# Optimization experiments

Hardware: AMD Instinct MI355X
Metric: run time of the kernel (lower is better)

## Reference

```python
import jax, jax.numpy as jnp
import numpy as np

RADIUS = 0.8
NSAMPLE = 32
EPS = 1e-5  # BatchNorm eps


def _bn(x, gamma, beta, axes):
    # BatchNorm (training-mode batch statistics), channel dim kept via broadcasting
    m = jnp.mean(x, axis=axes, keepdims=True)
    v = jnp.var(x, axis=axes, keepdims=True)
    return (x - m) * jax.lax.rsqrt(v + EPS) * gamma + beta


def setup_inputs() -> dict:
    key = jax.random.key(0)
    ks = jax.random.split(key, 6)
    B, N, P, C, COUT = 4, 8192, 2048, 128, 256
    ffps_xyz = jax.random.uniform(ks[0], (B, P, 3), dtype=jnp.float32) * 2.0 - 1.0
    backbone_xyz = jax.random.uniform(ks[1], (B, N, 3), dtype=jnp.float32) * 2.0 - 1.0
    backbone_features = jax.random.normal(ks[2], (B, C, N), dtype=jnp.float32)
    w_shift = jax.random.normal(ks[3], (3, 3), dtype=jnp.float32) * 0.1
    gamma_shift = jnp.ones((3,), jnp.float32)
    beta_shift = jnp.zeros((3,), jnp.float32)
    w_mlp = jax.random.normal(ks[4], (COUT, 3 + C), dtype=jnp.float32) * 0.05
    gamma_mlp = jnp.ones((COUT,), jnp.float32)
    beta_mlp = jnp.zeros((COUT,), jnp.float32)
    return {
        "ffps_xyz": ffps_xyz,
        "backbone_xyz": backbone_xyz,
        "backbone_features": backbone_features,
        "w_shift": w_shift,
        "gamma_shift": gamma_shift,
        "beta_shift": beta_shift,
        "w_mlp": w_mlp,
        "gamma_mlp": gamma_mlp,
        "beta_mlp": beta_mlp,
    }


def reference(ffps_xyz, backbone_xyz, backbone_features,
              w_shift, gamma_shift, beta_shift,
              w_mlp, gamma_mlp, beta_mlp):
    B, P, _ = ffps_xyz.shape
    N = backbone_xyz.shape[1]

    # ---- shift_layer: Conv1d(3->3, k=1, no bias) + BN1d + ReLU on (B,3,P) ----
    x = jnp.einsum('oc,bpc->bop', w_shift, ffps_xyz)                  # (B,3,P)
    x = _bn(x, gamma_shift[None, :, None], beta_shift[None, :, None], (0, 2))
    new_xyz = jax.nn.relu(x).transpose(0, 2, 1)                       # (B,P,3) query centers

    # ---- QueryAndGroup: ball query (radius, nsample), use_xyz=True ----
    d2 = jnp.sum((new_xyz[:, :, None, :] - backbone_xyz[:, None, :, :]) ** 2, -1)  # (B,P,N)
    within = d2 < (RADIUS * RADIUS)
    # pick the first NSAMPLE in-radius indices (CUDA ball_query semantics)
    keyv = jnp.where(within, jnp.arange(N, dtype=jnp.int32), jnp.int32(N))
    negk, idx = jax.lax.top_k(-keyv, NSAMPLE)                          # smallest keys first
    valid = (-negk) < N
    idx = jnp.where(valid, idx, idx[..., :1])                          # pad with first found idx

    g_xyz = jnp.take_along_axis(backbone_xyz[:, None, :, :], idx[..., None], axis=2)
    g_xyz = g_xyz - new_xyz[:, :, None, :]                             # (B,P,S,3) recentered
    feats = backbone_features.transpose(0, 2, 1)                       # (B,N,C)
    g_f = jnp.take_along_axis(feats[:, None, :, :], idx[..., None], axis=2)  # (B,P,S,C)
    g = jnp.concatenate([g_xyz, g_f], axis=-1)                         # (B,P,S,3+C)

    # ---- mlp: 1x1 conv (3+C -> COUT, no bias) + BN + ReLU ----
    y = jnp.einsum('oc,bpsc->bops', w_mlp, g)                          # (B,COUT,P,S)
    y = _bn(y, gamma_mlp[None, :, None, None], beta_mlp[None, :, None, None], (0, 2, 3))
    y = jax.nn.relu(y)

    # ---- max-pool over neighbor axis, squeeze, transpose ----
    y = jnp.max(y, axis=3)                                             # (B,COUT,P)
    return y.transpose(0, 2, 1)                                        # (B,P,COUT)
```

## Files before the change

kernel.cpp:

```cpp
#include <hip/hip_runtime.h>
#include <math.h>

namespace {
constexpr int B    = 4;
constexpr int N    = 8192;
constexpr int P    = 2048;
constexpr int C    = 128;
constexpr int COUT = 256;
constexpr int NS   = 32;
constexpr int BP   = B * P;
constexpr int BPB  = 2;
constexpr int GRP  = 8;
constexpr int NBLK = BP / (BPB * GRP);

constexpr size_t OFF_FEATT = 0;
constexpr size_t OFF_WSWZ  = 8388608;
constexpr size_t OFF_SSLOT = 8470528;
constexpr size_t OFF_SUMS  = 8471040;
constexpr size_t OFF_NXF   = 8475136;
constexpr size_t OFF_IDX   = 8573440;
constexpr size_t OFF_YMAX  = 9622016;
constexpr size_t WS_NEED   = 18010624;
}

typedef short bf16x8 __attribute__((ext_vector_type(8)));
typedef float f32x4  __attribute__((ext_vector_type(4)));

typedef const __attribute__((address_space(1))) void gas_void;
typedef __attribute__((address_space(3))) void las_void;
#define GLOBAL_LOAD_LDS16(gp, lp) \
    __builtin_amdgcn_global_load_lds((gas_void*)(gp), (las_void*)(lp), 16, 0, 0)

__device__ inline unsigned short f2bf(float f) {
    unsigned u = __float_as_uint(f);
    unsigned r = u + 0x7fffu + ((u >> 16) & 1u);
    return (unsigned short)(r >> 16);
}

__global__ __launch_bounds__(256) void k_prep(const float* __restrict__ ffps,
                                              const float* __restrict__ wsh,
                                              double* __restrict__ sslot,
                                              float* __restrict__ sums) {
#pragma clang fp contract(off)
    int blk = blockIdx.x, t = threadIdx.x;
    if (blk == 8) {
        ((f32x4*)sums)[t & 127] = (f32x4){0.f, 0.f, 0.f, 0.f};
        return;
    }
    __shared__ double red[6][256];
    double w[9];
#pragma unroll
    for (int i = 0; i < 9; i++) w[i] = (double)wsh[i];
    double s[3] = {0, 0, 0}, sq[3] = {0, 0, 0};
#pragma unroll
    for (int i = 0; i < 4; i++) {
        int p = blk * 1024 + t + 256 * i;
        double f0 = (double)ffps[p * 3 + 0];
        double f1 = (double)ffps[p * 3 + 1];
        double f2 = (double)ffps[p * 3 + 2];
#pragma unroll
        for (int o = 0; o < 3; o++) {
            double xo = (w[o * 3 + 0] * f0 + w[o * 3 + 1] * f1) + w[o * 3 + 2] * f2;
            s[o] += xo;
            sq[o] += xo * xo;
        }
    }
#pragma unroll
    for (int o = 0; o < 3; o++) { red[o][t] = s[o]; red[3 + o][t] = sq[o]; }
    for (int off = 128; off > 0; off >>= 1) {
        __syncthreads();
        if (t < off) {
#pragma unroll
            for (int j = 0; j < 6; j++) red[j][t] += red[j][t + off];
        }
    }
    __syncthreads();
    if (t < 6) sslot[blk * 6 + t] = red[t][0];
}

__global__ __launch_bounds__(256) void k_front(const float* __restrict__ ffps,
                                               const float* __restrict__ bbxyz,
                                               const float* __restrict__ feat,
                                               const float* __restrict__ wsh,
                                               const float* __restrict__ gsh,
                                               const float* __restrict__ bsh,
                                               const float* __restrict__ wml,
                                               const double* __restrict__ sslot,
                                               unsigned short* __restrict__ featT,
                                               unsigned short* __restrict__ wswz,
                                               float* __restrict__ nxf,
                                               int* __restrict__ idxo) {
#pragma clang fp contract(off)
    int blk = blockIdx.x, t = threadIdx.x;
    if (blk >= 2048) {
        int rb = blk - 2048;
        if (rb < 2048) {
            __shared__ float tile[64][33];
            int tx = t & 31, ty = t >> 5;
            int n0 = (rb & 255) * 32, c0 = ((rb >> 8) & 1) * 64, b = rb >> 9;
            const float* src = feat + ((size_t)b * C + c0) * N + n0;
#pragma unroll
            for (int j = 0; j < 8; j++) tile[ty + 8 * j][tx] = src[(size_t)(ty + 8 * j) * N + tx];
            __syncthreads();
            int n = t >> 3;
            int k8 = (t & 7) * 8;
            unsigned vv[4];
#pragma unroll
            for (int i = 0; i < 4; i++) {
                unsigned lo = f2bf(tile[k8 + 2 * i][n]);
                unsigned hi = f2bf(tile[k8 + 2 * i + 1][n]);
                vv[i] = lo | (hi << 16);
            }
            *(int4*)&featT[((size_t)b * N + n0 + n) * C + c0 + k8] =
                make_int4((int)vv[0], (int)vv[1], (int)vv[2], (int)vv[3]);
        } else {
            int i = (rb - 2048) * 256 + t;
            int j = i & 7;
            int lane = (i >> 3) & 63;
            int rest = i >> 9;
            int ks = rest % 5, rt = rest / 5;
            int cout = rt * 16 + (lane & 15);
            int k = ks * 32 + (lane >> 4) * 8 + j;
            float v = 0.f;
            if (k < 128) v = wml[cout * 131 + 3 + k];
            else if (k < 131) v = wml[cout * 131 + (k - 128)];
            wswz[i] = f2bf(v);
        }
        return;
    }

    __shared__ double spar[6];
    if (t < 6) {
        double a = 0.0;
        for (int r = 0; r < 8; r++) a += sslot[r * 6 + t];
        spar[t] = a;
    }
    __syncthreads();
    int wv = t >> 6, lane = t & 63;
    int q = blk * 4 + wv;
    int b = q >> 11;
    double f0 = (double)ffps[q * 3 + 0];
    double f1 = (double)ffps[q * 3 + 1];
    double f2 = (double)ffps[q * 3 + 2];
    double qd[3];
#pragma unroll
    for (int o = 0; o < 3; o++) {
        double m  = spar[o] * (1.0 / 8192.0);
        double v  = spar[3 + o] * (1.0 / 8192.0) - m * m;
        double is = 1.0 / sqrt(v + 1e-5);
        double x  = ((double)wsh[o * 3 + 0] * f0 + (double)wsh[o * 3 + 1] * f1) +
                    (double)wsh[o * 3 + 2] * f2;
        double y  = ((x - m) * is) * (double)gsh[o] + (double)bsh[o];
        qd[o] = (y > 0.0) ? y : 0.0;
    }
    double qx = qd[0], qy = qd[1], qz = qd[2];
    if (lane == 0) {
        nxf[q * 3 + 0] = (float)qx;
        nxf[q * 3 + 1] = (float)qy;
        nxf[q * 3 + 2] = (float)qz;
    }
    const double R2 = 0.8 * 0.8;
    {
        double ex = fmax(fmax(qx - 1.0, -1.0 - qx), 0.0);
        double ey = fmax(fmax(qy - 1.0, -1.0 - qy), 0.0);
        double ez = fmax(fmax(qz - 1.0, -1.0 - qz), 0.0);
        if (ex * ex + ey * ey + ez * ez >= R2) {
            if (lane < NS) idxo[q * NS + lane] = 0;
            return;
        }
    }
    const float* base = bbxyz + (size_t)b * N * 3;
    int found = 0, firstn = -1;

    float X0[8], Y0[8], Z0[8], X1[8], Y1[8], Z1[8], X2[8], Y2[8], Z2[8];

    auto loadb = [&](float (&XX)[8], float (&YY)[8], float (&ZZ)[8], int it) {
#pragma unroll
        for (int j = 0; j < 8; j++) {
            int n = it * 512 + j * 64 + lane;
            XX[j] = base[n * 3 + 0];
            YY[j] = base[n * 3 + 1];
            ZZ[j] = base[n * 3 + 2];
        }
    };
    auto proc = [&](float (&XX)[8], float (&YY)[8], float (&ZZ)[8], int it) {
#pragma clang fp contract(off)
#pragma unroll
        for (int j = 0; j < 8; j++) {
            int n = it * 512 + j * 64 + lane;
            double dx = qx - (double)XX[j];
            double dy = qy - (double)YY[j];
            double dz = qz - (double)ZZ[j];
            double d2 = (dx * dx + dy * dy) + dz * dz;
            bool within = d2 < R2;
            unsigned long long mask = __ballot(within);
            if (firstn < 0 && mask != 0ull) firstn = (n - lane) + (__ffsll(mask) - 1);
            if (within) {
                int rank = found + __popcll(mask & ((1ull << lane) - 1ull));
                if (rank < NS) idxo[q * NS + rank] = n;
            }
            found += __popcll(mask);
        }
    };

    loadb(X0, Y0, Z0, 0);
    loadb(X1, Y1, Z1, 1);
    loadb(X2, Y2, Z2, 2);

    for (int itb = 0; itb < 16; itb += 3) {
        proc(X0, Y0, Z0, itb);
        if (found >= NS) break;
        loadb(X0, Y0, Z0, (itb + 3 < 16) ? itb + 3 : 0);
        if (itb + 1 >= 16) break;
        proc(X1, Y1, Z1, itb + 1);
        if (found >= NS) break;
        loadb(X1, Y1, Z1, (itb + 4 < 16) ? itb + 4 : 0);
        if (itb + 2 >= 16) break;
        proc(X2, Y2, Z2, itb + 2);
        if (found >= NS) break;
        loadb(X2, Y2, Z2, (itb + 5 < 16) ? itb + 5 : 0);
    }
    if (found < NS) {
        int padv = (found == 0) ? 0 : firstn;
        if (lane >= found && lane < NS) idxo[q * NS + lane] = padv;
    }
}

__global__ __launch_bounds__(256, 2) void k_mlp_mfma(
        const float* __restrict__ bbxyz,
        const unsigned short* __restrict__ featT,
        const unsigned short* __restrict__ wswz,
        const float* __restrict__ nxf,
        const int* __restrict__ idx,
        float* __restrict__ ymax,
        float* __restrict__ sums) {
    __shared__ alignas(16) unsigned short G[2][4 * 4 * 64 * 8];
    int t = threadIdx.x, lane = t & 63, w = t >> 6;
    int q = lane >> 4, c16 = lane & 15;
    int blk = blockIdx.x;
    int bpbase = blk * (BPB * GRP);
    const bf16x8* wp = (const bf16x8*)wswz;

    bf16x8 wreg[5][4];
#pragma unroll
    for (int ks = 0; ks < 5; ks++)
#pragma unroll
        for (int nt = 0; nt < 4; nt++)
            wreg[ks][nt] = wp[((w * 4 + nt) * 5 + ks) * 64 + lane];

    int n_cur[4], n_nxt[4], n_nx2[4];
#pragma unroll
    for (int mt = 0; mt < 4; mt++)
        n_cur[mt] = idx[(bpbase + (mt >> 1)) * NS + (mt & 1) * 16 + c16];
#pragma unroll
    for (int mt = 0; mt < 4; mt++)
        n_nxt[mt] = idx[(bpbase + BPB + (mt >> 1)) * NS + (mt & 1) * 16 + c16];
    {
        int bp = bpbase + (w >> 1);
        const unsigned short* row = featT + ((size_t)(bp >> 11) * N + n_cur[w]) * C + q * 8;
#pragma unroll
        for (int ks = 0; ks < 4; ks++)
            GLOBAL_LOAD_LDS16(row + ks * 32, &G[0][(w * 4 + ks) * 512]);
    }

    float smA[4] = {0.f, 0.f, 0.f, 0.f}, sqA[4] = {0.f, 0.f, 0.f, 0.f};

    for (int g = 0; g < GRP; g++) {
        int buf = g & 1;
        int bp0 = bpbase + g * BPB;
        if (g + 2 < GRP) {
#pragma unroll
            for (int mt = 0; mt < 4; mt++)
                n_nx2[mt] = idx[(bp0 + 2 * BPB + (mt >> 1)) * NS + (mt & 1) * 16 + c16];
        }
        __syncthreads();
        if (g + 1 < GRP) {
            int bp = bp0 + BPB + (w >> 1);
            const unsigned short* row = featT + ((size_t)(bp >> 11) * N + n_nxt[w]) * C + q * 8;
#pragma unroll
            for (int ks = 0; ks < 4; ks++)
                GLOBAL_LOAD_LDS16(row + ks * 32, &G[buf ^ 1][(w * 4 + ks) * 512]);
        }

        f32x4 acc[4][4];
#pragma unroll
        for (int mt = 0; mt < 4; mt++)
#pragma unroll
            for (int nt = 0; nt < 4; nt++) acc[mt][nt] = (f32x4){0.f, 0.f, 0.f, 0.f};

#pragma unroll
        for (int ks = 0; ks < 4; ks++) {
            bf16x8 ag[4];
#pragma unroll
            for (int mt = 0; mt < 4; mt++)
                ag[mt] = *(const bf16x8*)&G[buf][((mt * 4 + ks) * 64 + lane) * 8];
#pragma unroll
            for (int nt = 0; nt < 4; nt++)
#pragma unroll
                for (int mt = 0; mt < 4; mt++)
                    acc[mt][nt] = __builtin_amdgcn_mfma_f32_16x16x32_bf16(ag[mt], wreg[ks][nt], acc[mt][nt], 0, 0, 0);
        }
        {
            bf16x8 agx[4];
#pragma unroll
            for (int mt = 0; mt < 4; mt++) {
                int bp = bp0 + (mt >> 1);
                unsigned u01 = 0, u23 = 0;
                if (q == 0) {
                    const float* src = bbxyz + ((size_t)(bp >> 11) * N + n_cur[mt]) * 3;
                    const float* ctr = nxf + bp * 3;
                    u01 = (unsigned)f2bf(src[0] - ctr[0]) | ((unsigned)f2bf(src[1] - ctr[1]) << 16);
                    u23 = (unsigned)f2bf(src[2] - ctr[2]);
                }
                union { int4 i; bf16x8 h; } u;
                u.i = make_int4((int)u01, (int)u23, 0, 0);
                agx[mt] = u.h;
            }
#pragma unroll
            for (int nt = 0; nt < 4; nt++)
#pragma unroll
                for (int mt = 0; mt < 4; mt++)
                    acc[mt][nt] = __builtin_amdgcn_mfma_f32_16x16x32_bf16(agx[mt], wreg[4][nt], acc[mt][nt], 0, 0, 0);
        }

#pragma unroll
        for (int pm = 0; pm < BPB; pm++) {
            int bp = bp0 + pm;
#pragma unroll
            for (int nt = 0; nt < 4; nt++) {
                f32x4 a = acc[2 * pm][nt], c = acc[2 * pm + 1][nt];
                float mx = fmaxf(fmaxf(fmaxf(a[0], a[1]), fmaxf(a[2], a[3])),
                                 fmaxf(fmaxf(c[0], c[1]), fmaxf(c[2], c[3])));
                smA[nt] += ((a[0] + a[1]) + (a[2] + a[3])) + ((c[0] + c[1]) + (c[2] + c[3]));
                sqA[nt] += ((a[0] * a[0] + a[1] * a[1]) + (a[2] * a[2] + a[3] * a[3])) +
                           ((c[0] * c[0] + c[1] * c[1]) + (c[2] * c[2] + c[3] * c[3]));
                mx = fmaxf(mx, __shfl_xor(mx, 16, 64));
                mx = fmaxf(mx, __shfl_xor(mx, 32, 64));
                if (q == 0)
                    ymax[(size_t)bp * COUT + w * 64 + nt * 16 + c16] = mx;
            }
        }
#pragma unroll
        for (int mt = 0; mt < 4; mt++) { n_cur[mt] = n_nxt[mt]; n_nxt[mt] = n_nx2[mt]; }
    }

#pragma unroll
    for (int nt = 0; nt < 4; nt++) {
        float sm = smA[nt], sq = sqA[nt];
        sm += __shfl_xor(sm, 16, 64);
        sm += __shfl_xor(sm, 32, 64);
        sq += __shfl_xor(sq, 16, 64);
        sq += __shfl_xor(sq, 32, 64);
        if (q == 0) {
            int cout = w * 64 + nt * 16 + c16;
            atomicAdd(&sums[cout], sm);
            atomicAdd(&sums[256 + cout], sq);
        }
    }
}

__global__ __launch_bounds__(256) void k_final(const float* __restrict__ ymax,
                                               const float* __restrict__ sums,
                                               const float* __restrict__ gam,
                                               const float* __restrict__ bet,
                                               float* __restrict__ out) {
    __shared__ float sa[256], sb[256];
    int t = threadIdx.x;
    {
        double sm = (double)sums[t], sq = (double)sums[256 + t];
        double mean = sm * (1.0 / 262144.0);
        double var = sq * (1.0 / 262144.0) - mean * mean;
        double a = (double)gam[t] / sqrt(var + 1e-5);
        sa[t] = (float)a;
        sb[t] = (float)((double)bet[t] - mean * a);
    }
    __syncthreads();
    int i = blockIdx.x * 256 + t;
    int c0 = (t & 63) * 4;
    f32x4 y = *(const f32x4*)&ymax[(size_t)i * 4];
    f32x4 r;
#pragma unroll
    for (int j = 0; j < 4; j++) r[j] = fmaxf(sa[c0 + j] * y[j] + sb[c0 + j], 0.f);
    *(f32x4*)&out[(size_t)i * 4] = r;
}

extern "C" void kernel_launch(void* const* d_in, const int* in_sizes, int n_in,
                              void* d_out, int out_size, void* d_ws, size_t ws_size,
                              hipStream_t stream) {
    const float* ffps  = (const float*)d_in[0];
    const float* bbxyz = (const float*)d_in[1];
    const float* feat  = (const float*)d_in[2];
    const float* wsh   = (const float*)d_in[3];
    const float* gsh   = (const float*)d_in[4];
    const float* bsh   = (const float*)d_in[5];
    const float* wml   = (const float*)d_in[6];
    const float* gml   = (const float*)d_in[7];
    const float* bml   = (const float*)d_in[8];
    float* out = (float*)d_out;
    char* ws = (char*)d_ws;
    if (ws_size < WS_NEED) return;

    unsigned short* featT = (unsigned short*)(ws + OFF_FEATT);
    unsigned short* wswz  = (unsigned short*)(ws + OFF_WSWZ);
    double*         sslot = (double*)(ws + OFF_SSLOT);
    float*          sums  = (float*)(ws + OFF_SUMS);
    float*          nxf   = (float*)(ws + OFF_NXF);
    int*            idx   = (int*)(ws + OFF_IDX);
    float*          ymax  = (float*)(ws + OFF_YMAX);

    k_prep<<<dim3(9), dim3(256), 0, stream>>>(ffps, wsh, sslot, sums);
    k_front<<<dim3(2048 + 2048 + 160), dim3(256), 0, stream>>>(
        ffps, bbxyz, feat, wsh, gsh, bsh, wml, sslot, featT, wswz, nxf, idx);
    k_mlp_mfma<<<dim3(NBLK), dim3(256), 0, stream>>>(bbxyz, featT, wswz, nxf, idx, ymax, sums);
    k_final<<<dim3(BP * COUT / 1024), dim3(256), 0, stream>>>(ymax, sums, gml, bml, out);
}
```

Baseline: 158.3 us.

## Precompute recentered bf16 neighbor xyz in ball query, drop gather in MLP

The ball-query kernel now writes the recentered, bf16-packed neighbor coordinates alongside each index, so the MLP kernel no longer gathers backbone xyz and center positions per sample. The MLP kernel also loads only the index each wave needs for its own feature row, and prefetches the packed xyz one group ahead. This removes dependent scattered loads and f2bf conversions from the MFMA loop. In exchange the front kernel does extra stores (8 bytes per sample) and the workspace grows.

```diff
diff --git a/kernel.cpp b/kernel.cpp
--- a/kernel.cpp
+++ b/kernel.cpp
@@ -17,10 +17,10 @@
 constexpr size_t OFF_WSWZ  = 8388608;
 constexpr size_t OFF_SSLOT = 8470528;
 constexpr size_t OFF_SUMS  = 8471040;
-constexpr size_t OFF_NXF   = 8475136;
-constexpr size_t OFF_IDX   = 8573440;
-constexpr size_t OFF_YMAX  = 9622016;
-constexpr size_t WS_NEED   = 18010624;
+constexpr size_t OFF_IDX   = 8475136;
+constexpr size_t OFF_GX    = 9523712;
+constexpr size_t OFF_YMAX  = 11620864;
+constexpr size_t WS_NEED   = 20009472;
 }
 
 typedef short bf16x8 __attribute__((ext_vector_type(8)));
@@ -88,8 +88,8 @@
                                                const double* __restrict__ sslot,
                                                unsigned short* __restrict__ featT,
                                                unsigned short* __restrict__ wswz,
-                                               float* __restrict__ nxf,
-                                               int* __restrict__ idxo) {
+                                               int* __restrict__ idxo,
+                                               uint2* __restrict__ gxo) {
 #pragma clang fp contract(off)
     int blk = blockIdx.x, t = threadIdx.x;
     if (blk >= 2048) {
@@ -154,22 +154,23 @@
         qd[o] = (y > 0.0) ? y : 0.0;
     }
     double qx = qd[0], qy = qd[1], qz = qd[2];
-    if (lane == 0) {
-        nxf[q * 3 + 0] = (float)qx;
-        nxf[q * 3 + 1] = (float)qy;
-        nxf[q * 3 + 2] = (float)qz;
-    }
+    float cfx = (float)qx, cfy = (float)qy, cfz = (float)qz;
+    const float* base = bbxyz + (size_t)b * N * 3;
     const double R2 = 0.8 * 0.8;
     {
         double ex = fmax(fmax(qx - 1.0, -1.0 - qx), 0.0);
         double ey = fmax(fmax(qy - 1.0, -1.0 - qy), 0.0);
         double ez = fmax(fmax(qz - 1.0, -1.0 - qz), 0.0);
         if (ex * ex + ey * ey + ez * ez >= R2) {
-            if (lane < NS) idxo[q * NS + lane] = 0;
+            if (lane < NS) {
+                idxo[q * NS + lane] = 0;
+                float rx = base[0] - cfx, ry = base[1] - cfy, rz = base[2] - cfz;
+                unsigned u01 = (unsigned)f2bf(rx) | ((unsigned)f2bf(ry) << 16);
+                gxo[q * NS + lane] = make_uint2(u01, (unsigned)f2bf(rz));
+            }
             return;
         }
     }
-    const float* base = bbxyz + (size_t)b * N * 3;
     int found = 0, firstn = -1;
 
     float X0[8], Y0[8], Z0[8], X1[8], Y1[8], Z1[8], X2[8], Y2[8], Z2[8];
@@ -197,7 +198,12 @@
             if (firstn < 0 && mask != 0ull) firstn = (n - lane) + (__ffsll(mask) - 1);
             if (within) {
                 int rank = found + __popcll(mask & ((1ull << lane) - 1ull));
-                if (rank < NS) idxo[q * NS + rank] = n;
+                if (rank < NS) {
+                    idxo[q * NS + rank] = n;
+                    float rx = XX[j] - cfx, ry = YY[j] - cfy, rz = ZZ[j] - cfz;
+                    unsigned u01 = (unsigned)f2bf(rx) | ((unsigned)f2bf(ry) << 16);
+                    gxo[q * NS + rank] = make_uint2(u01, (unsigned)f2bf(rz));
+                }
             }
             found += __popcll(mask);
         }
@@ -222,16 +228,22 @@
     }
     if (found < NS) {
         int padv = (found == 0) ? 0 : firstn;
-        if (lane >= found && lane < NS) idxo[q * NS + lane] = padv;
+        if (lane >= found && lane < NS) {
+            idxo[q * NS + lane] = padv;
+            float rx = base[padv * 3 + 0] - cfx;
+            float ry = base[padv * 3 + 1] - cfy;
+            float rz = base[padv * 3 + 2] - cfz;
+            unsigned u01 = (unsigned)f2bf(rx) | ((unsigned)f2bf(ry) << 16);
+            gxo[q * NS + lane] = make_uint2(u01, (unsigned)f2bf(rz));
+        }
     }
 }
 
 __global__ __launch_bounds__(256, 2) void k_mlp_mfma(
-        const float* __restrict__ bbxyz,
         const unsigned short* __restrict__ featT,
         const unsigned short* __restrict__ wswz,
-        const float* __restrict__ nxf,
         const int* __restrict__ idx,
+        const uint2* __restrict__ gxyz,
         float* __restrict__ ymax,
         float* __restrict__ sums) {
     __shared__ alignas(16) unsigned short G[2][4 * 4 * 64 * 8];
@@ -248,16 +260,18 @@
         for (int nt = 0; nt < 4; nt++)
             wreg[ks][nt] = wp[((w * 4 + nt) * 5 + ks) * 64 + lane];
 
-    int n_cur[4], n_nxt[4], n_nx2[4];
-#pragma unroll
-    for (int mt = 0; mt < 4; mt++)
-        n_cur[mt] = idx[(bpbase + (mt >> 1)) * NS + (mt & 1) * 16 + c16];
-#pragma unroll
-    for (int mt = 0; mt < 4; mt++)
-        n_nxt[mt] = idx[(bpbase + BPB + (mt >> 1)) * NS + (mt & 1) * 16 + c16];
+    int sOff = (w >> 1) * NS + (w & 1) * 16 + c16;
+    size_t fb = (size_t)(bpbase >> 11) * N * C;
+
+    int nS0 = idx[bpbase * NS + sOff];
+    int nS1 = idx[(bpbase + BPB) * NS + sOff];
+    uint2 gx_c[4] = {}, gx_n[4] = {};
+    if (q == 0)
+#pragma unroll
+        for (int mt = 0; mt < 4; mt++)
+            gx_c[mt] = gxyz[(bpbase + (mt >> 1)) * NS + (mt & 1) * 16 + c16];
     {
-        int bp = bpbase + (w >> 1);
-        const unsigned short* row = featT + ((size_t)(bp >> 11) * N + n_cur[w]) * C + q * 8;
+        const unsigned short* row = featT + fb + (size_t)nS0 * C + q * 8;
 #pragma unroll
         for (int ks = 0; ks < 4; ks++)
             GLOBAL_LOAD_LDS16(row + ks * 32, &G[0][(w * 4 + ks) * 512]);
@@ -268,19 +282,18 @@
     for (int g = 0; g < GRP; g++) {
         int buf = g & 1;
         int bp0 = bpbase + g * BPB;
-        if (g + 2 < GRP) {
-#pragma unroll
-            for (int mt = 0; mt < 4; mt++)
-                n_nx2[mt] = idx[(bp0 + 2 * BPB + (mt >> 1)) * NS + (mt & 1) * 16 + c16];
-        }
         __syncthreads();
         if (g + 1 < GRP) {
-            int bp = bp0 + BPB + (w >> 1);
-            const unsigned short* row = featT + ((size_t)(bp >> 11) * N + n_nxt[w]) * C + q * 8;
+            const unsigned short* row = featT + fb + (size_t)nS1 * C + q * 8;
 #pragma unroll
             for (int ks = 0; ks < 4; ks++)
                 GLOBAL_LOAD_LDS16(row + ks * 32, &G[buf ^ 1][(w * 4 + ks) * 512]);
-        }
+            if (q == 0)
+#pragma unroll
+                for (int mt = 0; mt < 4; mt++)
+                    gx_n[mt] = gxyz[(bp0 + BPB + (mt >> 1)) * NS + (mt & 1) * 16 + c16];
+        }
+        if (g + 2 < GRP) nS0 = idx[(bp0 + 2 * BPB) * NS + sOff];
 
         f32x4 acc[4][4];
 #pragma unroll
@@ -304,16 +317,9 @@
             bf16x8 agx[4];
 #pragma unroll
             for (int mt = 0; mt < 4; mt++) {
-                int bp = bp0 + (mt >> 1);
-                unsigned u01 = 0, u23 = 0;
-                if (q == 0) {
-                    const float* src = bbxyz + ((size_t)(bp >> 11) * N + n_cur[mt]) * 3;
-                    const float* ctr = nxf + bp * 3;
-                    u01 = (unsigned)f2bf(src[0] - ctr[0]) | ((unsigned)f2bf(src[1] - ctr[1]) << 16);
-                    u23 = (unsigned)f2bf(src[2] - ctr[2]);
-                }
                 union { int4 i; bf16x8 h; } u;
-                u.i = make_int4((int)u01, (int)u23, 0, 0);
+                u.i = make_int4(q == 0 ? (int)gx_c[mt].x : 0,
+                                q == 0 ? (int)gx_c[mt].y : 0, 0, 0);
                 agx[mt] = u.h;
             }
 #pragma unroll
@@ -340,8 +346,9 @@
                     ymax[(size_t)bp * COUT + w * 64 + nt * 16 + c16] = mx;
             }
         }
-#pragma unroll
-        for (int mt = 0; mt < 4; mt++) { n_cur[mt] = n_nxt[mt]; n_nxt[mt] = n_nx2[mt]; }
+        nS1 = nS0;
+#pragma unroll
+        for (int mt = 0; mt < 4; mt++) gx_c[mt] = gx_n[mt];
     }
 
 #pragma unroll
@@ -404,13 +411,13 @@
     unsigned short* wswz  = (unsigned short*)(ws + OFF_WSWZ);
     double*         sslot = (double*)(ws + OFF_SSLOT);
     float*          sums  = (float*)(ws + OFF_SUMS);
-    float*          nxf   = (float*)(ws + OFF_NXF);
     int*            idx   = (int*)(ws + OFF_IDX);
+    uint2*          gx    = (uint2*)(ws + OFF_GX);
     float*          ymax  = (float*)(ws + OFF_YMAX);
 
     k_prep<<<dim3(9), dim3(256), 0, stream>>>(ffps, wsh, sslot, sums);
     k_front<<<dim3(2048 + 2048 + 160), dim3(256), 0, stream>>>(
-        ffps, bbxyz, feat, wsh, gsh, bsh, wml, sslot, featT, wswz, nxf, idx);
-    k_mlp_mfma<<<dim3(NBLK), dim3(256), 0, stream>>>(bbxyz, featT, wswz, nxf, idx, ymax, sums);
+        ffps, bbxyz, feat, wsh, gsh, bsh, wml, sslot, featT, wswz, idx, gx);
+    k_mlp_mfma<<<dim3(NBLK), dim3(256), 0, stream>>>(featT, wswz, idx, gx, ymax, sums);
     k_final<<<dim3(BP * COUT / 1024), dim3(256), 0, stream>>>(ymax, sums, gml, bml, out);
 }
```

Measured after the change: 156.1 us. No clear change (-1.4%).
